# Kernel optimization log

Hardware: AMD Instinct MI355X
Metric: run time of the kernel (lower is better)

## Reference

```python
import math
import jax, jax.numpy as jnp
import numpy as np

# ---- static config (from init_kwargs) ----
B = 4
FH, FW = 480, 640          # frame size
NSEM = 16
C_OBS = 4 + NSEM           # 20 obs channels (rgb, depth, sem)
C_FEAT = 1 + NSEM          # 17 splatted feature channels
RES = 5.0                  # map resolution cm
VR = 100                   # vision range (cells)
MAXH, MINH = 72, -8        # int(360/5), int(-40/5)
HZ = MAXH - MINH           # 80 height bins
MAP_CELLS = 480            # (4800//2)//5
AGENT_H = 88.0             # camera_height*100
FOV = 79.0
N = FH * FW                # du_scale = 1
MAP_T, EXP_T, CAT_T = 1.0, 1.0, 5.0
DEG = 57.29577951308232
MIN_Z, MAX_Z = 13, 25      # int(25/5 - min_h), int((agent_h+1)/5 - min_h)
X1, X2 = 190, 290          # map crop window
Y1, Y2 = 240, 340


def setup_inputs() -> dict:
    key = jax.random.key(0)
    k1, k2, k3, k4, k5 = jax.random.split(key, 5)
    obs = jax.random.uniform(k1, (B, C_OBS, FH, FW), jnp.float32)
    obs = obs.at[:, 3].multiply(500.0)  # depth channel in cm
    pose_obs = jax.random.normal(k2, (B, 3), jnp.float32) * 0.1
    maps_last = jax.random.uniform(k3, (B, C_OBS, MAP_CELLS, MAP_CELLS), jnp.float32)
    poses_last = jax.random.normal(k4, (B, 3), jnp.float32) * 0.3 \
        + jnp.array([12.0, 12.0, 0.0], jnp.float32)  # near map center (meters, deg)
    sh = jax.random.normal(k5, (B, N, 4), jnp.float32) * 0.1  # SH coeffs per point
    return {"obs": obs, "pose_obs": pose_obs, "maps_last": maps_last,
            "poses_last": poses_last, "sh": sh}


def _affine_grid(theta, H, W):
    # align_corners=True affine grid; theta: (bs, 2, 3) -> (bs, H, W, 2)
    ys = jnp.linspace(-1.0, 1.0, H, dtype=jnp.float32)
    xs = jnp.linspace(-1.0, 1.0, W, dtype=jnp.float32)
    gx, gy = jnp.meshgrid(xs, ys)                       # (H, W)
    base = jnp.stack([gx, gy, jnp.ones_like(gx)], -1)   # (H, W, 3)
    return jnp.einsum('bij,hwj->bhwi', theta, base)


def _grid_sample(img, grid):
    # bilinear, zeros padding, align_corners=True. img: (bs,C,H,W), grid: (bs,H,W,2)
    Bs, C, H, W = img.shape
    x = (grid[..., 0] + 1.0) * (W - 1) / 2.0
    y = (grid[..., 1] + 1.0) * (H - 1) / 2.0
    x0 = jnp.floor(x); y0 = jnp.floor(y)
    x1 = x0 + 1.0; y1 = y0 + 1.0

    def one(img_b, xb, yb, x0b, y0b, x1b, y1b):
        def tap(ix, iy):
            valid = ((ix >= 0) & (ix < W) & (iy >= 0) & (iy < H)).astype(img_b.dtype)
            ic = jnp.clip(ix, 0, W - 1).astype(jnp.int32)
            jc = jnp.clip(iy, 0, H - 1).astype(jnp.int32)
            return img_b[:, jc, ic] * valid[None]        # (C,H,W)
        w00 = (x1b - xb) * (y1b - yb)
        w01 = (xb - x0b) * (y1b - yb)
        w10 = (x1b - xb) * (yb - y0b)
        w11 = (xb - x0b) * (yb - y0b)
        return (tap(x0b, y0b) * w00[None] + tap(x1b, y0b) * w01[None]
                + tap(x0b, y1b) * w10[None] + tap(x1b, y1b) * w11[None])

    return jax.vmap(one)(img, x, y, x0, y0, x1, y1)


def _splat_one(feat_b, coords_b):
    # trilinear scatter-add splat (du.splat_feat_nd). feat_b: (C_FEAT, N), coords_b: (3, N) in [-1,1]
    GD = (VR, VR, HZ)
    grid = jnp.zeros((C_FEAT, VR * VR * HZ), jnp.float32)
    pos = [coords_b[d] * GD[d] / 2.0 + GD[d] / 2.0 for d in range(3)]
    for ix in ((0, 0, 0), (0, 0, 1), (0, 1, 0), (0, 1, 1),
               (1, 0, 0), (1, 0, 1), (1, 1, 0), (1, 1, 1)):
        idx = jnp.zeros((N,), jnp.float32)
        w = jnp.ones((N,), jnp.float32)
        for d in range(3):
            p = jnp.floor(pos[d]) + ix[d]
            safe = ((p > 0) & (p < GD[d])).astype(jnp.float32)
            w = w * (1.0 - jnp.abs(pos[d] - p)) * safe
            idx = idx * GD[d] + p * safe
        grid = grid.at[:, idx.astype(jnp.int32)].add(feat_b * w[None, :])
    return grid


def _forward(obs, pose_obs, maps_last, poses_last, sh):
    bs = obs.shape[0]
    depth = obs[:, 3]                                   # (bs, FH, FW)

    # --- point cloud from depth (du.get_point_cloud_from_z_t) ---
    f = (FW / 2.0) / math.tan(math.radians(FOV / 2.0))
    xc = (FW - 1) / 2.0
    zc = (FH - 1) / 2.0
    gx = jnp.arange(FW, dtype=jnp.float32)
    gz = jnp.arange(FH - 1, -1, -1, dtype=jnp.float32)
    X = (gx[None, None, :] - xc) * depth / f
    Z = (gz[None, :, None] - zc) * depth / f
    # camera view transform (elev=0 -> identity rot, z += agent_h) then
    # shift_loc pose transform (angle pi/2 -> identity rot, x += vr*res//2)
    x_s = X + float(VR * int(RES) // 2)
    y_s = depth
    z_s = Z + AGENT_H

    # --- normalize to [-1,1] voxel coords ---
    xn = (x_s / RES - float(VR // 2)) / VR * 2.0
    yn = (y_s / RES - float(VR // 2)) / VR * 2.0
    zn = (z_s / RES - float((MAXH + MINH) // 2)) / (MAXH - MINH) * 2.0
    coords = jnp.stack([xn, yn, zn], axis=1).reshape(bs, 3, N)
    coords = jnp.clip(coords, -1.0, 1.0)

    # --- features (channel 0 = ones occupancy, rest = semantics; du_scale=1 so avgpool is identity) ---
    feat = jnp.concatenate(
        [jnp.ones((bs, 1, N), jnp.float32), obs[:, 4:].reshape(bs, NSEM, N)], axis=1)
    sh_mean = jnp.mean(sh, axis=2)                      # (bs, N)
    enh = feat * (1.0 + sh_mean[:, None, :])

    # --- voxel splat + round, swap the two xy grid dims (matches .transpose(2,3)) ---
    vox = jax.vmap(_splat_one)(enh, coords)
    vox = jnp.round(vox).reshape(bs, C_FEAT, VR, VR, HZ).transpose(0, 1, 3, 2, 4)

    # --- height projections ---
    agent_proj = vox[..., MIN_Z:MAX_Z].sum(-1)          # (bs, C_FEAT, VR, VR)
    all_proj = vox.sum(-1)
    fp_map_pred = jnp.clip(agent_proj[:, 0:1] / MAP_T, 0.0, 1.0)
    fp_exp_pred = jnp.clip(all_proj[:, 0:1] / EXP_T, 0.0, 1.0)

    # --- write into egocentric map ---
    av = jnp.zeros((bs, C_OBS, MAP_CELLS, MAP_CELLS), jnp.float32)
    av = av.at[:, 0:1, Y1:Y2, X1:X2].set(fp_map_pred)
    av = av.at[:, 1:2, Y1:Y2, X1:X2].set(fp_exp_pred)
    av = av.at[:, 4:, Y1:Y2, X1:X2].set(jnp.clip(agent_proj[:, 1:] / CAT_T, 0.0, 1.0))

    # --- pose integration ---
    t0 = poses_last[:, 2] / DEG
    y_new = poses_last[:, 1] + pose_obs[:, 0] * jnp.sin(t0) + pose_obs[:, 1] * jnp.cos(t0)
    x_new = poses_last[:, 0] + pose_obs[:, 0] * jnp.cos(t0) - pose_obs[:, 1] * jnp.sin(t0)
    t_new = poses_last[:, 2] + pose_obs[:, 2] * DEG
    t_new = jnp.fmod(t_new - 180.0, 360.0) + 180.0
    t_new = jnp.fmod(t_new + 180.0, 360.0) - 180.0
    current_poses = jnp.stack([x_new, y_new, t_new], axis=1)

    # --- spatial transform of egocentric map into allocentric frame ---
    stc = jax.lax.stop_gradient(current_poses)          # matches .clone().detach()
    half = float(MAP_CELLS // 2)                        # 240
    st_xy = -(stc[:, :2] * 100.0 / RES - half) / half
    st_t = (90.0 - stc[:, 2]) * (math.pi / 180.0)
    cos_t, sin_t = jnp.cos(st_t), jnp.sin(st_t)
    zeros = jnp.zeros_like(cos_t); ones = jnp.ones_like(cos_t)
    theta1 = jnp.stack([jnp.stack([cos_t, -sin_t, zeros], 1),
                        jnp.stack([sin_t, cos_t, zeros], 1)], 1)    # (bs,2,3)
    theta2 = jnp.stack([jnp.stack([ones, zeros, st_xy[:, 0]], 1),
                        jnp.stack([zeros, ones, st_xy[:, 1]], 1)], 1)
    rot_grid = _affine_grid(theta1, MAP_CELLS, MAP_CELLS)
    trans_grid = _affine_grid(theta2, MAP_CELLS, MAP_CELLS)
    rotated = _grid_sample(av, rot_grid)
    translated = _grid_sample(rotated, trans_grid)

    map_pred = jnp.maximum(maps_last, translated)
    # pose_pred aliases poses_last which is mutated in-place in torch -> equals current_poses
    return fp_map_pred, map_pred, current_poses, current_poses


def reference(obs, pose_obs, maps_last, poses_last, sh):
    return _forward(obs, pose_obs, maps_last, poses_last, sh)
```

## Files before the change

kernel.cpp:

```cpp
#include <hip/hip_runtime.h>
#include <math.h>

#define FHh 480
#define FWw 640
#define NPIX (FHh*FWw)
#define NSEMC 16
#define COBS 20
#define MAPC 480
#define VRc 100
#define HZc 80
#define MINZc 13
#define MAXZc 25
#define ZW 12
#define ZWP 13
#define OCCP 81
#define NB 4
#define NBINS_DIM 101
#define NBINS_ROW 101
#define COUNTS_PAD 40960
#define BANDMAX 600000
#define NTOT (NB*NPIX)

__global__ void pose_kernel(const float* __restrict__ pose_obs,
                            const float* __restrict__ poses_last,
                            float* __restrict__ out_p1,
                            float* __restrict__ out_p2,
                            float* __restrict__ params)
{
    int b = threadIdx.x;
    if (b >= NB) return;
    float pl0 = poses_last[b*3+0], pl1 = poses_last[b*3+1], pl2 = poses_last[b*3+2];
    float po0 = pose_obs[b*3+0],  po1 = pose_obs[b*3+1],  po2 = pose_obs[b*3+2];
    const float DEGf = 57.29577951308232f;
    float t0 = pl2 / DEGf;
    float s = sinf(t0), c = cosf(t0);
    float y_new = pl1 + po0*s + po1*c;
    float x_new = pl0 + po0*c - po1*s;
    float t_new = pl2 + po2*DEGf;
    t_new = fmodf(t_new - 180.0f, 360.0f) + 180.0f;
    t_new = fmodf(t_new + 180.0f, 360.0f) - 180.0f;
    out_p1[b*3+0]=x_new; out_p1[b*3+1]=y_new; out_p1[b*3+2]=t_new;
    out_p2[b*3+0]=x_new; out_p2[b*3+1]=y_new; out_p2[b*3+2]=t_new;
    float sx = -(((x_new*100.0f)/5.0f - 240.0f)/240.0f);
    float sy = -(((y_new*100.0f)/5.0f - 240.0f)/240.0f);
    float st_t = (90.0f - t_new) * 0.017453292519943295f;
    params[b*4+0] = cosf(st_t);
    params[b*4+1] = sinf(st_t);
    params[b*4+2] = sx;
    params[b*4+3] = sy;
}

__device__ __forceinline__ float4 pixel_pos(const float* __restrict__ obsb,
                                            const float* __restrict__ sh,
                                            int b, int n, float fconst)
{
    int col = n % FWw, row = n / FWw;
    float depth = obsb[3*NPIX + n];
    const float4 s4 = ((const float4*)sh)[(size_t)b*NPIX + n];
    float sm = (((s4.x + s4.y) + s4.z) + s4.w) / 4.0f;
    float factor = 1.0f + sm;

    float X = ((float)col - 319.5f) * depth / fconst;
    float Z = ((float)(FHh-1-row) - 239.5f) * depth / fconst;
    float x_s = X + 250.0f;
    float z_s = Z + 88.0f;
    float xn = (x_s/5.0f - 50.0f)/100.0f*2.0f;
    float yn = (depth/5.0f - 50.0f)/100.0f*2.0f;
    float zn = (z_s/5.0f - 32.0f)/80.0f*2.0f;
    xn = fminf(fmaxf(xn,-1.0f),1.0f);
    yn = fminf(fmaxf(yn,-1.0f),1.0f);
    zn = fminf(fmaxf(zn,-1.0f),1.0f);
    float pos0 = (xn*100.0f)/2.0f + 50.0f;
    float pos1 = (yn*100.0f)/2.0f + 50.0f;
    float pos2 = (zn*80.0f)/2.0f + 40.0f;
    return make_float4(pos0, pos1, pos2, factor);
}

__device__ __forceinline__ bool dim_ok(float p, int GD)
{
    int f = (int)floorf(p);
    float fr = p - (float)f;
    bool t0 = (f > 0) && (f < GD);
    bool t1 = (f + 1 < GD) && (fr > 0.0f);
    return t0 || t1;
}

__global__ __launch_bounds__(256)
void count_kernel(const float* __restrict__ obs,
                  const float* __restrict__ sh,
                  int* __restrict__ counts,
                  int* __restrict__ countsB,
                  float fconst)
{
    int g = blockIdx.x*blockDim.x + threadIdx.x;
    if (g >= NTOT) return;
    int b = g / NPIX, n = g % NPIX;
    const float* obsb = obs + (size_t)b*COBS*NPIX;
    float4 P = pixel_pos(obsb, sh, b, n, fconst);

    if (!(dim_ok(P.x, VRc) && dim_ok(P.y, VRc) && dim_ok(P.z, HZc))) return;
    int f0 = (int)floorf(P.x);
    int f1 = (int)floorf(P.y);
    int bid = (b*NBINS_DIM + f1)*NBINS_ROW + f0;
    atomicAdd(&counts[bid], 1);
    if (P.z > 12.0f && P.z < 25.0f) atomicAdd(&countsB[bid], 1);
}

__global__ void scan_kernel(int* __restrict__ base)
{
    int* cnt = base + (size_t)blockIdx.x * 2 * COUNTS_PAD;
    int* wrk = cnt + COUNTS_PAD;
    __shared__ int part[1024];
    int t = threadIdx.x;
    const int CHUNK = COUNTS_PAD / 1024;
    int bo = t*CHUNK;
    int s = 0;
    for (int k = 0; k < CHUNK; ++k) s += cnt[bo+k];
    part[t] = s;
    __syncthreads();
    for (int off = 1; off < 1024; off <<= 1) {
        int v = (t >= off) ? part[t-off] : 0;
        __syncthreads();
        part[t] += v;
        __syncthreads();
    }
    int run = part[t] - s;
    for (int k = 0; k < CHUNK; ++k) {
        int c = cnt[bo+k];
        cnt[bo+k] = run;
        wrk[bo+k] = run;
        run += c;
    }
}

__global__ __launch_bounds__(256)
void scatter_kernel(const float* __restrict__ obs,
                    const float* __restrict__ sh,
                    int* __restrict__ offsetsWork,
                    int* __restrict__ offsetsWorkB,
                    float4* __restrict__ payloadPos,
                    float4* __restrict__ bandPos,
                    float4* __restrict__ bandSem,
                    float fconst)
{
    int g = blockIdx.x*blockDim.x + threadIdx.x;
    if (g >= NTOT) return;
    int b = g / NPIX, n = g % NPIX;
    const float* obsb = obs + (size_t)b*COBS*NPIX;
    float4 P = pixel_pos(obsb, sh, b, n, fconst);

    if (!(dim_ok(P.x, VRc) && dim_ok(P.y, VRc) && dim_ok(P.z, HZc))) return;
    int f0 = (int)floorf(P.x);
    int f1 = (int)floorf(P.y);
    int bid = (b*NBINS_DIM + f1)*NBINS_ROW + f0;

    int dst = atomicAdd(&offsetsWork[bid], 1);
    if (dst < NTOT) payloadPos[dst] = P;

    if (P.z > 12.0f && P.z < 25.0f) {
        int dstB = atomicAdd(&offsetsWorkB[bid], 1);
        if (dstB < BANDMAX) {
            bandPos[dstB] = P;
            float4* bs = bandSem + (size_t)dstB*4;
            #pragma unroll
            for (int q = 0; q < 4; ++q) {
                float4 e;
                e.x = obsb[(4 + 4*q + 0)*NPIX + n] * P.w;
                e.y = obsb[(4 + 4*q + 1)*NPIX + n] * P.w;
                e.z = obsb[(4 + 4*q + 2)*NPIX + n] * P.w;
                e.w = obsb[(4 + 4*q + 3)*NPIX + n] * P.w;
                bs[q] = e;
            }
        }
    }
}

__global__ __launch_bounds__(256)
void gather_rows_kernel(const float4* __restrict__ payloadPos,
                        const int* __restrict__ offsets,
                        const float4* __restrict__ bandPos,
                        const float* __restrict__ bandSemF,
                        const int* __restrict__ offsetsB,
                        float* __restrict__ avwin,
                        float* __restrict__ fp_out)
{
    int j  = blockIdx.x >> 1;
    int i0 = (blockIdx.x & 1) * 50;
    int b  = blockIdx.y;
    int tid = threadIdx.x;

    __shared__ float accSem[50*NSEMC*ZWP];
    __shared__ float accOcc[50*OCCP];

    for (int k = tid; k < 50*NSEMC*ZWP; k += 256) accSem[k] = 0.0f;
    for (int k = tid; k < 50*OCCP; k += 256) accOcc[k] = 0.0f;
    __syncthreads();

    if (j >= 1) {
        int f0lo = (i0 == 0) ? 0 : (i0 - 1);
        int f0hi = i0 + 49;
        int tmin = (i0 == 0) ? 1 : i0;
        int cgrp = tid & 15;
        #pragma unroll
        for (int seg = 0; seg < 2; ++seg) {
            int f1r = j - 1 + seg;
            int rb = (b*NBINS_DIM + f1r)*NBINS_ROW;

            int s = offsets[rb + f0lo];
            int e = offsets[rb + f0hi + 1];
            if (s < 0) s = 0;
            if (e > NTOT) e = NTOT;
            for (int idx = s + tid; idx < e; idx += 256) {
                float4 P = payloadPos[idx];
                float wy = 1.0f - fabsf(P.y - (float)j);
                if (wy <= 0.0f) continue;
                int f0c = (int)floorf(P.x);
                int qA  = (int)floorf(P.z);
                #pragma unroll
                for (int di = 0; di < 2; ++di) {
                    int ti = f0c + di;
                    if (ti < tmin || ti > i0 + 49) continue;
                    float wx = 1.0f - fabsf(P.x - (float)ti);
                    if (wx <= 0.0f) continue;
                    float wxy = wx * wy;
                    int base = (ti - i0)*OCCP;
                    #pragma unroll
                    for (int dz = 0; dz < 2; ++dz) {
                        int q = qA + dz;
                        if (q < 1 || q > 79) continue;
                        float w = wxy * (1.0f - fabsf(P.z - (float)q));
                        if (w > 0.0f) atomicAdd(&accOcc[base + q], P.w * w);
                    }
                }
            }

            int sB = offsetsB[rb + f0lo];
            int eB = offsetsB[rb + f0hi + 1];
            if (sB < 0) sB = 0;
            if (eB > BANDMAX) eB = BANDMAX;
            for (int idx = sB + (tid >> 4); idx < eB; idx += 16) {
                float4 P = bandPos[idx];
                float wy = 1.0f - fabsf(P.y - (float)j);
                if (wy <= 0.0f) continue;
                float ev = bandSemF[(size_t)idx*16 + cgrp];
                int f0c = (int)floorf(P.x);
                int qA  = (int)floorf(P.z);
                #pragma unroll
                for (int di = 0; di < 2; ++di) {
                    int ti = f0c + di;
                    if (ti < tmin || ti > i0 + 49) continue;
                    float wx = 1.0f - fabsf(P.x - (float)ti);
                    if (wx <= 0.0f) continue;
                    float wxy = wx * wy;
                    int base = ((ti - i0)*NSEMC + cgrp)*ZWP - MINZc;
                    #pragma unroll
                    for (int dz = 0; dz < 2; ++dz) {
                        int q = qA + dz;
                        if (q < MINZc || q >= MAXZc) continue;
                        float w = wxy * (1.0f - fabsf(P.z - (float)q));
                        if (w > 0.0f) atomicAdd(&accSem[base + q], ev * w);
                    }
                }
            }
        }
    }
    __syncthreads();

    float* avb = avwin + (size_t)b*18*10000;
    int cell0 = j*100 + i0;

    for (int c = tid; c < 50; c += 256) {
        float agent = 0.0f, all = 0.0f;
        for (int z = 0; z < HZc; ++z) {
            float r = rintf(accOcc[c*OCCP + z]);
            all += r;
            if (z >= MINZc && z < MAXZc) agent += r;
        }
        float va = fminf(fmaxf(agent, 0.0f), 1.0f);
        avb[cell0 + c] = va;
        fp_out[(size_t)b*10000 + cell0 + c] = va;
        avb[10000 + cell0 + c] = fminf(fmaxf(all, 0.0f), 1.0f);
    }
    for (int t = tid; t < 50*NSEMC; t += 256) {
        int c = t >> 4, ch = t & 15;
        float s = 0.0f;
        #pragma unroll
        for (int z = 0; z < ZW; ++z) s += rintf(accSem[(c*NSEMC + ch)*ZWP + z]);
        avb[(2+ch)*10000 + cell0 + c] = fminf(fmaxf(s*0.2f, 0.0f), 1.0f);
    }
}

__device__ __forceinline__ float grid1d(int i) {
    return (float)(-1.0 + (double)i * (2.0/479.0));
}

__global__ void map_kernel(const float* __restrict__ maps_last,
                           const float* __restrict__ avwin,
                           const float* __restrict__ params,
                           float* __restrict__ map_out)
{
    int t = blockIdx.x*blockDim.x + threadIdx.x;
    if (t >= NB*MAPC*MAPC) return;
    int w = t % MAPC;
    int h = (t / MAPC) % MAPC;
    int b = t / (MAPC*MAPC);
    float ct = params[b*4+0], st = params[b*4+1];
    float sx = params[b*4+2], sy = params[b*4+3];

    float xg = grid1d(w) + sx;
    float yg = grid1d(h) + sy;
    float xt = ((xg + 1.0f)*479.0f)/2.0f;
    float yt = ((yg + 1.0f)*479.0f)/2.0f;
    float xf = floorf(xt), yf = floorf(yt);

    float acc[18];
    #pragma unroll
    for (int k=0;k<18;k++) acc[k]=0.0f;
    const float* avb = avwin + (size_t)b*18*10000;

    #pragma unroll
    for (int oy=0; oy<2; ++oy) {
        #pragma unroll
        for (int ox=0; ox<2; ++ox) {
            float qx = xf + (float)ox, qy = yf + (float)oy;
            if (!(qx >= 0.0f && qx < 480.0f && qy >= 0.0f && qy < 480.0f)) continue;
            float wo = (ox ? (xt - xf) : (xf + 1.0f - xt))
                     * (oy ? (yt - yf) : (yf + 1.0f - yt));
            int oxi = (int)qx, oyi = (int)qy;
            float gxr = grid1d(oxi), gyr = grid1d(oyi);
            float xr = ct*gxr - st*gyr;
            float yr = st*gxr + ct*gyr;
            float xp = ((xr + 1.0f)*479.0f)/2.0f;
            float yp = ((yr + 1.0f)*479.0f)/2.0f;
            float xpf = floorf(xp), ypf = floorf(yp);
            float R[18];
            #pragma unroll
            for (int k=0;k<18;k++) R[k]=0.0f;
            #pragma unroll
            for (int iy=0; iy<2; ++iy) {
                #pragma unroll
                for (int ix=0; ix<2; ++ix) {
                    float rx = xpf + (float)ix, ry = ypf + (float)iy;
                    if (!(rx >= 0.0f && rx < 480.0f && ry >= 0.0f && ry < 480.0f)) continue;
                    int rxi = (int)rx, ryi = (int)ry;
                    if (ryi < 240 || ryi >= 340 || rxi < 190 || rxi >= 290) continue;
                    float wi = (ix ? (xp - xpf) : (xpf + 1.0f - xp))
                             * (iy ? (yp - ypf) : (ypf + 1.0f - yp));
                    const float* p = avb + (ryi-240)*VRc + (rxi-190);
                    #pragma unroll
                    for (int k=0;k<18;k++) R[k] += wi * p[k*10000];
                }
            }
            #pragma unroll
            for (int k=0;k<18;k++) acc[k] += wo * R[k];
        }
    }

    #pragma unroll
    for (int c=0;c<COBS;c++) {
        size_t o = (((size_t)b*COBS + c)*MAPC + h)*MAPC + w;
        float tv = (c==0) ? acc[0] : (c==1) ? acc[1] : (c>=4) ? acc[c-2] : 0.0f;
        map_out[o] = fmaxf(maps_last[o], tv);
    }
}

extern "C" void kernel_launch(void* const* d_in, const int* in_sizes, int n_in,
                              void* d_out, int out_size, void* d_ws, size_t ws_size,
                              hipStream_t stream)
{
    const float* obs        = (const float*)d_in[0];
    const float* pose_obs   = (const float*)d_in[1];
    const float* maps_last  = (const float*)d_in[2];
    const float* poses_last = (const float*)d_in[3];
    const float* sh         = (const float*)d_in[4];
    float* out = (float*)d_out;

    float* fp_out  = out;
    float* map_out = out + 40000;
    float* poses1  = out + 40000 + 18432000;
    float* poses2  = poses1 + 12;

    float* params = (float*)d_ws;
    float* avwin  = params + 16;

    float4* payloadPos   = (float4*)map_out;
    int*    counts       = (int*)(map_out + 4915200);
    int*    offsetsWork  = counts + COUNTS_PAD;
    int*    countsB      = counts + 2*COUNTS_PAD;
    int*    offsetsWorkB = counts + 3*COUNTS_PAD;
    float4* bandPos      = (float4*)(map_out + 4915200 + 4*COUNTS_PAD);
    float4* bandSem      = (float4*)(map_out + 4915200 + 4*COUNTS_PAD + (size_t)BANDMAX*4);

    double rad = 39.5 * 0.017453292519943295;
    float fconst = (float)(320.0 / tan(rad));

    hipLaunchKernelGGL(pose_kernel, dim3(1), dim3(64), 0, stream,
                       pose_obs, poses_last, poses1, poses2, params);

    hipMemsetAsync(counts, 0, (size_t)4*COUNTS_PAD*sizeof(int), stream);

    hipLaunchKernelGGL(count_kernel, dim3((NTOT+255)/256), dim3(256), 0, stream,
                       obs, sh, counts, countsB, fconst);

    hipLaunchKernelGGL(scan_kernel, dim3(2), dim3(1024), 0, stream, counts);

    hipLaunchKernelGGL(scatter_kernel, dim3((NTOT+255)/256), dim3(256), 0, stream,
                       obs, sh, offsetsWork, offsetsWorkB,
                       payloadPos, bandPos, bandSem, fconst);

    hipLaunchKernelGGL(gather_rows_kernel, dim3(200, NB), dim3(256), 0, stream,
                       payloadPos, counts, bandPos, (const float*)bandSem, countsB,
                       avwin, fp_out);

    hipLaunchKernelGGL(map_kernel, dim3((NB*MAPC*MAPC+255)/256), dim3(256), 0, stream,
                       maps_last, avwin, params, map_out);
}
```

Before: 907.4 us.

## Split gather into quarter-row blocks of 512 threads with prefetched band loads

The gather kernel now assigns each block a 25-cell quarter of a map row instead of half a row. It runs 512 threads per block and launches twice as many blocks, which raises parallelism and shrinks shared-memory accumulators. The band-semantic loop gains a software prefetch of the next point's position and feature, so load latency overlaps the atomic accumulation. The cost is that more points near block boundaries get read by two blocks, and the added prefetch registers could limit occupancy.

```diff
diff --git a/kernel.cpp b/kernel.cpp
--- a/kernel.cpp
+++ b/kernel.cpp
@@ -20,6 +20,7 @@
 #define COUNTS_PAD 40960
 #define BANDMAX 600000
 #define NTOT (NB*NPIX)
+#define QW 25
 
 __global__ void pose_kernel(const float* __restrict__ pose_obs,
                             const float* __restrict__ poses_last,
@@ -175,7 +176,7 @@
     }
 }
 
-__global__ __launch_bounds__(256)
+__global__ __launch_bounds__(512, 4)
 void gather_rows_kernel(const float4* __restrict__ payloadPos,
                         const int* __restrict__ offsets,
                         const float4* __restrict__ bandPos,
@@ -184,22 +185,23 @@
                         float* __restrict__ avwin,
                         float* __restrict__ fp_out)
 {
-    int j  = blockIdx.x >> 1;
-    int i0 = (blockIdx.x & 1) * 50;
+    int j  = blockIdx.x >> 2;
+    int i0 = (blockIdx.x & 3) * QW;
     int b  = blockIdx.y;
     int tid = threadIdx.x;
 
-    __shared__ float accSem[50*NSEMC*ZWP];
-    __shared__ float accOcc[50*OCCP];
-
-    for (int k = tid; k < 50*NSEMC*ZWP; k += 256) accSem[k] = 0.0f;
-    for (int k = tid; k < 50*OCCP; k += 256) accOcc[k] = 0.0f;
+    __shared__ float accSem[QW*NSEMC*ZWP];
+    __shared__ float accOcc[QW*OCCP];
+
+    for (int k = tid; k < QW*NSEMC*ZWP; k += 512) accSem[k] = 0.0f;
+    for (int k = tid; k < QW*OCCP; k += 512) accOcc[k] = 0.0f;
     __syncthreads();
 
     if (j >= 1) {
         int f0lo = (i0 == 0) ? 0 : (i0 - 1);
-        int f0hi = i0 + 49;
+        int f0hi = i0 + QW - 1;
         int tmin = (i0 == 0) ? 1 : i0;
+        int tmax = i0 + QW - 1;
         int cgrp = tid & 15;
         #pragma unroll
         for (int seg = 0; seg < 2; ++seg) {
@@ -210,7 +212,7 @@
             int e = offsets[rb + f0hi + 1];
             if (s < 0) s = 0;
             if (e > NTOT) e = NTOT;
-            for (int idx = s + tid; idx < e; idx += 256) {
+            for (int idx = s + tid; idx < e; idx += 512) {
                 float4 P = payloadPos[idx];
                 float wy = 1.0f - fabsf(P.y - (float)j);
                 if (wy <= 0.0f) continue;
@@ -219,7 +221,7 @@
                 #pragma unroll
                 for (int di = 0; di < 2; ++di) {
                     int ti = f0c + di;
-                    if (ti < tmin || ti > i0 + 49) continue;
+                    if (ti < tmin || ti > tmax) continue;
                     float wx = 1.0f - fabsf(P.x - (float)ti);
                     if (wx <= 0.0f) continue;
                     float wxy = wx * wy;
@@ -238,29 +240,43 @@
             int eB = offsetsB[rb + f0hi + 1];
             if (sB < 0) sB = 0;
             if (eB > BANDMAX) eB = BANDMAX;
-            for (int idx = sB + (tid >> 4); idx < eB; idx += 16) {
-                float4 P = bandPos[idx];
+            int idx = sB + (tid >> 4);
+            float4 P; float ev;
+            bool have = idx < eB;
+            if (have) {
+                P = bandPos[idx];
+                ev = bandSemF[(size_t)idx*16 + cgrp];
+            }
+            while (have) {
+                int nidx = idx + 32;
+                bool nhave = nidx < eB;
+                float4 Pn = P; float evn = ev;
+                if (nhave) {
+                    Pn = bandPos[nidx];
+                    evn = bandSemF[(size_t)nidx*16 + cgrp];
+                }
                 float wy = 1.0f - fabsf(P.y - (float)j);
-                if (wy <= 0.0f) continue;
-                float ev = bandSemF[(size_t)idx*16 + cgrp];
-                int f0c = (int)floorf(P.x);
-                int qA  = (int)floorf(P.z);
-                #pragma unroll
-                for (int di = 0; di < 2; ++di) {
-                    int ti = f0c + di;
-                    if (ti < tmin || ti > i0 + 49) continue;
-                    float wx = 1.0f - fabsf(P.x - (float)ti);
-                    if (wx <= 0.0f) continue;
-                    float wxy = wx * wy;
-                    int base = ((ti - i0)*NSEMC + cgrp)*ZWP - MINZc;
+                if (wy > 0.0f) {
+                    int f0c = (int)floorf(P.x);
+                    int qA  = (int)floorf(P.z);
                     #pragma unroll
-                    for (int dz = 0; dz < 2; ++dz) {
-                        int q = qA + dz;
-                        if (q < MINZc || q >= MAXZc) continue;
-                        float w = wxy * (1.0f - fabsf(P.z - (float)q));
-                        if (w > 0.0f) atomicAdd(&accSem[base + q], ev * w);
+                    for (int di = 0; di < 2; ++di) {
+                        int ti = f0c + di;
+                        if (ti < tmin || ti > tmax) continue;
+                        float wx = 1.0f - fabsf(P.x - (float)ti);
+                        if (wx <= 0.0f) continue;
+                        float wxy = wx * wy;
+                        int base = ((ti - i0)*NSEMC + cgrp)*ZWP - MINZc;
+                        #pragma unroll
+                        for (int dz = 0; dz < 2; ++dz) {
+                            int q = qA + dz;
+                            if (q < MINZc || q >= MAXZc) continue;
+                            float w = wxy * (1.0f - fabsf(P.z - (float)q));
+                            if (w > 0.0f) atomicAdd(&accSem[base + q], ev * w);
+                        }
                     }
                 }
+                idx = nidx; have = nhave; P = Pn; ev = evn;
             }
         }
     }
@@ -269,7 +285,7 @@
     float* avb = avwin + (size_t)b*18*10000;
     int cell0 = j*100 + i0;
 
-    for (int c = tid; c < 50; c += 256) {
+    for (int c = tid; c < QW; c += 512) {
         float agent = 0.0f, all = 0.0f;
         for (int z = 0; z < HZc; ++z) {
             float r = rintf(accOcc[c*OCCP + z]);
@@ -281,7 +297,7 @@
         fp_out[(size_t)b*10000 + cell0 + c] = va;
         avb[10000 + cell0 + c] = fminf(fmaxf(all, 0.0f), 1.0f);
     }
-    for (int t = tid; t < 50*NSEMC; t += 256) {
+    for (int t = tid; t < QW*NSEMC; t += 512) {
         int c = t >> 4, ch = t & 15;
         float s = 0.0f;
         #pragma unroll
@@ -408,7 +424,7 @@
                        obs, sh, offsetsWork, offsetsWorkB,
                        payloadPos, bandPos, bandSem, fconst);
 
-    hipLaunchKernelGGL(gather_rows_kernel, dim3(200, NB), dim3(256), 0, stream,
+    hipLaunchKernelGGL(gather_rows_kernel, dim3(400, NB), dim3(512), 0, stream,
                        payloadPos, counts, bandPos, (const float*)bandSem, countsB,
                        avwin, fp_out);
 
```

New measurement: 1.114 ms. 1.23x slower.
